# Kernel tuning notes

Hardware: AMD Instinct MI355X
Metric: run time of the kernel (lower is better)

## Reference

```python
import jax, jax.numpy as jnp
import numpy as np

B, T, D_IN, D, K, H, BAND = 4, 1536, 512, 512, 2, 8, 24
DH = D // H
ALPHA, BETA, EPS = 6.0, 0.5, 1e-5


def _ln(x, g, b):
    m = x.mean(-1, keepdims=True)
    v = ((x - m) ** 2).mean(-1, keepdims=True)
    return (x - m) / jnp.sqrt(v + EPS) * g + b


def setup_inputs() -> dict:
    key = jax.random.key(0)
    ks = jax.random.split(key, 16)
    sc = 0.02
    inp = {
        "x_m": jax.random.normal(ks[0], (B, T, D_IN), jnp.float32),
        "A": jax.random.uniform(ks[1], (B, T, K), jnp.float32),
        "W_in": jax.random.normal(ks[2], (D_IN, D), jnp.float32) * sc,
        "b_in": jnp.zeros((D,), jnp.float32),
        "ln_q_g": jnp.ones((D,), jnp.float32), "ln_q_b": jnp.zeros((D,), jnp.float32),
        "ln_kv_g": jnp.ones((D,), jnp.float32), "ln_kv_b": jnp.zeros((D,), jnp.float32),
        "Wq": jax.random.normal(ks[3], (D, D), jnp.float32) * sc,
        "bq": jnp.zeros((D,), jnp.float32),
        "Wk": jax.random.normal(ks[4], (D, D), jnp.float32) * sc,
        "bk": jnp.zeros((D,), jnp.float32),
        "Wv": jax.random.normal(ks[5], (D, D), jnp.float32) * sc,
        "bv": jnp.zeros((D,), jnp.float32),
        "Wo": jax.random.normal(ks[6], (D, D), jnp.float32) * sc,
        "bo": jnp.zeros((D,), jnp.float32),
        "ln_f_g": jnp.ones((D,), jnp.float32), "ln_f_b": jnp.zeros((D,), jnp.float32),
        "W1": jax.random.normal(ks[7], (D, 4 * D), jnp.float32) * sc,
        "b1": jnp.zeros((4 * D,), jnp.float32),
        "W2": jax.random.normal(ks[8], (4 * D, D), jnp.float32) * sc,
        "b2": jnp.zeros((D,), jnp.float32),
        "ln_s_g": jnp.ones((D,), jnp.float32), "ln_s_b": jnp.zeros((D,), jnp.float32),
        "spk_tags": jax.random.normal(ks[9], (K, D), jnp.float32) / np.sqrt(D),
    }
    return inp


def reference(x_m, A, W_in, b_in, ln_q_g, ln_q_b, ln_kv_g, ln_kv_b,
              Wq, bq, Wk, bk, Wv, bv, Wo, bo,
              ln_f_g, ln_f_b, W1, b1, W2, b2, ln_s_g, ln_s_b, spk_tags):
    X = x_m @ W_in + b_in                      # [B,T,D]
    W_hat = jax.nn.sigmoid(ALPHA * (A - BETA))  # [B,T,K] sigmoid gating

    # banded additive mask (|i-j| <= BAND allowed)
    idx = jnp.arange(T)
    allowed = jnp.abs(idx[:, None] - idx[None, :]) <= BAND
    mask = jnp.where(allowed, 0.0, -jnp.inf).astype(X.dtype)  # [T,T]

    # K/V come from the (shared) mixed memory X
    KV = _ln(X, ln_kv_g, ln_kv_b)
    k_p = (KV @ Wk + bk).reshape(B, T, H, DH)
    v_p = (KV @ Wv + bv).reshape(B, T, H, DH)

    streams = []
    for kk in range(K):
        Xk = X * W_hat[..., kk:kk + 1]
        Q = _ln(Xk, ln_q_g, ln_q_b)
        q = (Q @ Wq + bq).reshape(B, T, H, DH)
        scores = jnp.einsum('bthd,bshd->bhts', q, k_p) / np.sqrt(DH) + mask
        p = jax.nn.softmax(scores, axis=-1)
        y = jnp.einsum('bhts,bshd->bthd', p, v_p).reshape(B, T, D) @ Wo + bo
        y = Xk + y                              # residual after attention
        h = _ln(y, ln_f_g, ln_f_b)
        h = jax.nn.gelu(h @ W1 + b1, approximate=False) @ W2 + b2
        out_k = y + h + spk_tags[kk]            # ffn residual + speaker tag
        out_k = _ln(out_k, ln_s_g, ln_s_b)      # per-stream LayerNorm
        streams.append(out_k)
    return jnp.concatenate(streams, axis=1)    # [B, K*T, D]
```

## Files before the change

### kernel.cpp

```cpp
#include <hip/hip_runtime.h>
#include <hip/hip_bf16.h>
#include <math.h>

#define B_    4
#define T_    1536
#define DIN_  512
#define D_    512
#define K_    2
#define H_    8
#define BAND_ 24
#define DH_   64
#define M_    (B_*T_)
#define M2_   (2*M_)
#define ALPHA_ 6.0f
#define BETA_  0.5f
#define EPS_   1e-5f

using bf8  = __attribute__((ext_vector_type(8))) short;
using f32x4 = __attribute__((ext_vector_type(4))) float;

__device__ __forceinline__ void async_copy16(const void* g, void* l) {
  __builtin_amdgcn_global_load_lds(
      (const __attribute__((address_space(1))) unsigned int*)g,
      (__attribute__((address_space(3))) unsigned int*)l, 16, 0, 0);
}

__device__ __forceinline__ short f2bf(float v) {
  __hip_bfloat16 h = (__hip_bfloat16)v;
  return *(short*)&h;
}
__device__ __forceinline__ float bf2f(short s) {
  union { unsigned u; float f; } c;
  c.u = ((unsigned)(unsigned short)s) << 16;
  return c.f;
}
__device__ __forceinline__ int swz64(int row, int col) {
  return (col & ~63) | ((((col >> 3) ^ row) & 7) << 3) | (col & 7);
}
__device__ __forceinline__ float fast_gelu(float x) {
  const float t = fmaf(0.1029504013f, x * x, 2.3021170686f);
  const float e = __builtin_amdgcn_exp2f(x * t);
  const float r = __builtin_amdgcn_rcpf(e + 1.0f);
  return fmaf(-x, r, x);
}

template<int BM, int BN, int NI, int NJ, int FLAGS>
__global__ __launch_bounds__(256) void gemm_bt_t(
    const short* __restrict__ A, const short* __restrict__ Bt,
    const float* __restrict__ bias, const void* __restrict__ res,
    void* __restrict__ Cout, int M, int N, int Kd, int gx) {
  __shared__ short lA[BM * 64];
  __shared__ short lB[BN * 64];
  const int gy   = gridDim.x / gx;
  const int xcd  = blockIdx.x & 7;
  const int seq  = blockIdx.x >> 3;
  const int rpx  = gy >> 3;
  const int by   = xcd * rpx + seq / gx;
  const int bx   = seq % gx;
  const int tid  = threadIdx.x;
  const int wave = tid >> 6, lane = tid & 63;
  const int block_m = by * BM, block_n = bx * BN;
  const int wm = (wave & 1) * (BM / 2), wn = (wave >> 1) * (BN / 2);
  const int l15 = lane & 15, quad = lane >> 4, l7 = lane & 7;
  f32x4 acc[NI][NJ] = {};

  for (int k0 = 0; k0 < Kd; k0 += 64) {
    __syncthreads();
#pragma unroll
    for (int i = 0; i < BM / 32; ++i) {
      const int cb = wave * (BM * 2) + i * 64;
      const int c  = cb + lane;
      async_copy16(A + (size_t)(block_m + (c >> 3)) * Kd + k0 + (c & 7) * 8,
                   &lA[cb * 8]);
    }
#pragma unroll
    for (int i = 0; i < BN / 32; ++i) {
      const int cb = wave * (BN * 2) + i * 64;
      const int c  = cb + lane;
      async_copy16(Bt + (size_t)(block_n + (c >> 3)) * Kd + k0 + (c & 7) * 8,
                   &lB[cb * 8]);
    }
    __syncthreads();
#pragma unroll
    for (int ks = 0; ks < 2; ++ks) {
      bf8 af[NI], bfr[NJ];
#pragma unroll
      for (int i = 0; i < NI; ++i)
        af[i] = *(const bf8*)&lA[(wm + i * 16 + l15) * 64 + (((ks * 4 + quad) ^ l7) << 3)];
#pragma unroll
      for (int j = 0; j < NJ; ++j)
        bfr[j] = *(const bf8*)&lB[(wn + j * 16 + l15) * 64 + (((ks * 4 + quad) ^ l7) << 3)];
#pragma unroll
      for (int i = 0; i < NI; ++i)
#pragma unroll
        for (int j = 0; j < NJ; ++j)
          acc[i][j] = __builtin_amdgcn_mfma_f32_16x16x32_bf16(af[i], bfr[j], acc[i][j], 0, 0, 0);
    }
  }

#pragma unroll
  for (int i = 0; i < NI; ++i) {
    const int mbase = block_m + wm + i * 16 + (lane >> 4) * 4;
#pragma unroll
    for (int j = 0; j < NJ; ++j) {
      const int col = block_n + wn + j * 16 + l15;
      const float bb = bias[col];
#pragma unroll
      for (int r = 0; r < 4; ++r) {
        const int row = mbase + r;
        const size_t idx = (size_t)row * N + col;
        float v = acc[i][j][r] + bb;
        if constexpr (FLAGS & 8)  v += bf2f(((const short*)res)[idx]);
        if constexpr (FLAGS & 16) v += ((const float*)res)[idx];
        if constexpr (FLAGS & 1)  v = fast_gelu(v);
        if constexpr (FLAGS & 2) {
          const int oc = (FLAGS & 4) ? swz64(row, col) : col;
          ((short*)Cout)[(size_t)row * N + oc] = f2bf(v);
        } else {
          ((float*)Cout)[idx] = v;
        }
      }
    }
  }
}

__global__ __launch_bounds__(256) void tconv_k(const float* __restrict__ W,
                                               short* __restrict__ Wt, int K, int N) {
  __shared__ float s[32][33];
  const int tx = threadIdx.x & 31, ty = threadIdx.x >> 5;
  const int k0 = blockIdx.y * 32, n0 = blockIdx.x * 32;
#pragma unroll
  for (int r = 0; r < 4; ++r)
    s[ty * 4 + r][tx] = W[(size_t)(k0 + ty * 4 + r) * N + n0 + tx];
  __syncthreads();
#pragma unroll
  for (int r = 0; r < 4; ++r) {
    const int n = n0 + ty * 4 + r;
    Wt[(size_t)n * K + swz64(n, k0 + tx)] = f2bf(s[tx][ty * 4 + r]);
  }
}

__global__ void cvt_k(const float* __restrict__ x, short* __restrict__ y, int n) {
  const int i = blockIdx.x * blockDim.x + threadIdx.x;
  if (i < n) {
    const int row = i >> 9, col = i & 511;
    y[((size_t)row << 9) | swz64(row, col)] = f2bf(x[i]);
  }
}

__global__ void concat2_k(const float* __restrict__ a, const float* __restrict__ b,
                          float* __restrict__ o, int n) {
  const int i = blockIdx.x * blockDim.x + threadIdx.x;
  if (i < n) o[i] = a[i];
  else if (i < 2 * n) o[i] = b[i - n];
}

__device__ __forceinline__ float block_sum(float s, float* red, int tid) {
  red[tid] = s; __syncthreads();
  for (int o = 128; o > 0; o >>= 1) {
    if (tid < o) red[tid] += red[tid + o];
    __syncthreads();
  }
  float r = red[0];
  __syncthreads();
  return r;
}

__global__ __launch_bounds__(256) void ln_bf_k(const short* __restrict__ in,
                                               const float* __restrict__ g,
                                               const float* __restrict__ b,
                                               short* __restrict__ out) {
  __shared__ float red[256];
  const int row = blockIdx.x, tid = threadIdx.x;
  const short2 xv = *(const short2*)&in[(size_t)row * D_ + 2 * tid];
  const float v0 = bf2f(xv.x), v1 = bf2f(xv.y);
  const float mean = block_sum(v0 + v1, red, tid) * (1.0f / D_);
  const float d0 = v0 - mean, d1 = v1 - mean;
  const float var = block_sum(d0 * d0 + d1 * d1, red, tid) * (1.0f / D_);
  const float inv = rsqrtf(var + EPS_);
  const float2 gg = *(const float2*)&g[2 * tid];
  const float2 bb = *(const float2*)&b[2 * tid];
  short2 o;
  o.x = f2bf(d0 * inv * gg.x + bb.x);
  o.y = f2bf(d1 * inv * gg.y + bb.y);
  *(short2*)&out[(size_t)row * D_ + swz64(row, 2 * tid)] = o;
}

__global__ __launch_bounds__(256) void scale_ln_k(
    const short* __restrict__ X, const float* __restrict__ Ain,
    const float* __restrict__ g, const float* __restrict__ b,
    short* __restrict__ Xk, short* __restrict__ out) {
  __shared__ float red[256];
  const int row = blockIdx.x, tid = threadIdx.x;
  const int kk = row / M_, rm = row % M_;
  const float a = Ain[(size_t)rm * K_ + kk];
  const float w = __builtin_amdgcn_rcpf(1.0f + __expf(-ALPHA_ * (a - BETA_)));
  const short2 xv = *(const short2*)&X[(size_t)rm * D_ + 2 * tid];
  const float v0 = bf2f(xv.x) * w, v1 = bf2f(xv.y) * w;
  short2 xo; xo.x = f2bf(v0); xo.y = f2bf(v1);
  *(short2*)&Xk[(size_t)row * D_ + 2 * tid] = xo;
  const float mean = block_sum(v0 + v1, red, tid) * (1.0f / D_);
  const float d0 = v0 - mean, d1 = v1 - mean;
  const float var = block_sum(d0 * d0 + d1 * d1, red, tid) * (1.0f / D_);
  const float inv = rsqrtf(var + EPS_);
  const float2 gg = *(const float2*)&g[2 * tid];
  const float2 bb = *(const float2*)&b[2 * tid];
  short2 o;
  o.x = f2bf(d0 * inv * gg.x + bb.x);
  o.y = f2bf(d1 * inv * gg.y + bb.y);
  *(short2*)&out[(size_t)row * D_ + swz64(row, 2 * tid)] = o;
}

__global__ __launch_bounds__(256) void final_ln_k(
    const float* __restrict__ t2, const float* __restrict__ tags,
    const float* __restrict__ g, const float* __restrict__ b,
    float* __restrict__ out) {
  __shared__ float red[256];
  const int row = blockIdx.x, tid = threadIdx.x;
  const int kk = row / M_, rm = row % M_;
  const int bb = rm / T_, t = rm % T_;
  const size_t orow = (size_t)bb * (K_ * T_) + (size_t)kk * T_ + t;
  const float v0 = t2[(size_t)row * D_ + tid]       + tags[(size_t)kk * D_ + tid];
  const float v1 = t2[(size_t)row * D_ + tid + 256] + tags[(size_t)kk * D_ + tid + 256];
  const float mean = block_sum(v0 + v1, red, tid) * (1.0f / D_);
  const float d0 = v0 - mean, d1 = v1 - mean;
  const float var = block_sum(d0 * d0 + d1 * d1, red, tid) * (1.0f / D_);
  const float inv = rsqrtf(var + EPS_);
  out[orow * D_ + tid]       = d0 * inv * g[tid]       + b[tid];
  out[orow * D_ + tid + 256] = d1 * inv * g[tid + 256] + b[tid + 256];
}

#define QT_  64
#define KT_  (QT_ + 2 * BAND_)
#define SKQ_ 72
#define STV_ 136
__global__ __launch_bounds__(256) void attn_mfma_k(
    const short* __restrict__ q, const short* __restrict__ KVp,
    short* __restrict__ out) {
  __shared__ short sK[KT_ * SKQ_];
  __shared__ short sQ[QT_ * SKQ_];
  __shared__ short sVt[DH_ * STV_];
  __shared__ short sP[4][16 * SKQ_];
  const int t0 = blockIdx.x * QT_;
  const int h  = blockIdx.y;
  const int z  = blockIdx.z;
  const int b  = z % B_;
  const int tid = threadIdx.x;
  const int wave = tid >> 6, lane = tid & 63;
  const int rr = tid >> 5, c2 = tid & 31;

  for (int r0 = 0; r0 < KT_; r0 += 8) {
    const int r = r0 + rr;
    const int s = t0 - BAND_ + r;
    short2 kv = {0, 0}, vv = {0, 0};
    if (s >= 0 && s < T_) {
      const size_t g = (size_t)(b * T_ + s) * (2 * D_) + h * DH_ + c2 * 2;
      kv = *(const short2*)&KVp[g];
      vv = *(const short2*)&KVp[g + D_];
    }
    *(short2*)&sK[r * SKQ_ + c2 * 2] = kv;
    sVt[(c2 * 2)     * STV_ + r] = vv.x;
    sVt[(c2 * 2 + 1) * STV_ + r] = vv.y;
  }
  for (int r0 = 0; r0 < QT_; r0 += 8) {
    const int r = r0 + rr;
    const size_t g = (size_t)(z * T_ + t0 + r) * D_ + h * DH_ + c2 * 2;
    *(short2*)&sQ[r * SKQ_ + c2 * 2] = *(const short2*)&q[g];
  }
  __syncthreads();

  const int qg  = wave * 16;
  const int l15 = lane & 15, quad = lane >> 4;

  bf8 qa0 = *(const bf8*)&sQ[(qg + l15) * SKQ_ + quad * 8];
  bf8 qa1 = *(const bf8*)&sQ[(qg + l15) * SKQ_ + 32 + quad * 8];
  f32x4 acc[4];
#pragma unroll
  for (int j = 0; j < 4; ++j) {
    const bf8 kb0 = *(const bf8*)&sK[(qg + j * 16 + l15) * SKQ_ + quad * 8];
    const bf8 kb1 = *(const bf8*)&sK[(qg + j * 16 + l15) * SKQ_ + 32 + quad * 8];
    f32x4 z4 = {0.f, 0.f, 0.f, 0.f};
    acc[j] = __builtin_amdgcn_mfma_f32_16x16x32_bf16(qa0, kb0, z4, 0, 0, 0);
    acc[j] = __builtin_amdgcn_mfma_f32_16x16x32_bf16(qa1, kb1, acc[j], 0, 0, 0);
  }

#pragma unroll
  for (int reg = 0; reg < 4; ++reg) {
    const int i = quad * 4 + reg;
    float sc[4];
    float mx = -1e30f;
#pragma unroll
    for (int j = 0; j < 4; ++j) {
      const int c = j * 16 + l15;
      const int s = t0 + qg - BAND_ + c;
      const int rel = c - i;
      const bool valid = (rel >= 0) && (rel <= 2 * BAND_) && (s >= 0) && (s < T_);
      sc[j] = valid ? acc[j][reg] * 0.125f : -1e30f;
      mx = fmaxf(mx, sc[j]);
    }
    for (int o = 1; o < 16; o <<= 1) mx = fmaxf(mx, __shfl_xor(mx, o));
    float p[4], se = 0.0f;
#pragma unroll
    for (int j = 0; j < 4; ++j) {
      p[j] = (sc[j] > -1e29f) ? __expf(sc[j] - mx) : 0.0f;
      se += p[j];
    }
    for (int o = 1; o < 16; o <<= 1) se += __shfl_xor(se, o);
    const float inv = __builtin_amdgcn_rcpf(se);
#pragma unroll
    for (int j = 0; j < 4; ++j)
      sP[wave][i * SKQ_ + j * 16 + l15] = f2bf(p[j] * inv);
  }

  const bf8 pa0 = *(const bf8*)&sP[wave][l15 * SKQ_ + quad * 8];
  const bf8 pa1 = *(const bf8*)&sP[wave][l15 * SKQ_ + 32 + quad * 8];
  f32x4 oacc[4] = {};
#pragma unroll
  for (int dt = 0; dt < 4; ++dt) {
    const bf8 vb0 = *(const bf8*)&sVt[(dt * 16 + l15) * STV_ + qg + quad * 8];
    const bf8 vb1 = *(const bf8*)&sVt[(dt * 16 + l15) * STV_ + qg + 32 + quad * 8];
    oacc[dt] = __builtin_amdgcn_mfma_f32_16x16x32_bf16(pa0, vb0, oacc[dt], 0, 0, 0);
    oacc[dt] = __builtin_amdgcn_mfma_f32_16x16x32_bf16(pa1, vb1, oacc[dt], 0, 0, 0);
  }
#pragma unroll
  for (int dt = 0; dt < 4; ++dt)
#pragma unroll
    for (int reg = 0; reg < 4; ++reg) {
      const int i = quad * 4 + reg;
      const int row = t0 + qg + i;
      const int col = h * DH_ + dt * 16 + l15;
      out[(size_t)(z * T_ + row) * D_ + swz64(row, col)] = f2bf(oacc[dt][reg]);
    }
}

extern "C" void kernel_launch(void* const* d_in, const int* in_sizes, int n_in,
                              void* d_out, int out_size, void* d_ws, size_t ws_size,
                              hipStream_t stream) {
  const float* x_m    = (const float*)d_in[0];
  const float* A      = (const float*)d_in[1];
  const float* W_in   = (const float*)d_in[2];
  const float* b_in   = (const float*)d_in[3];
  const float* ln_q_g = (const float*)d_in[4];
  const float* ln_q_b = (const float*)d_in[5];
  const float* ln_kv_g= (const float*)d_in[6];
  const float* ln_kv_b= (const float*)d_in[7];
  const float* Wq     = (const float*)d_in[8];
  const float* bq     = (const float*)d_in[9];
  const float* Wk     = (const float*)d_in[10];
  const float* bk     = (const float*)d_in[11];
  const float* Wv     = (const float*)d_in[12];
  const float* bv     = (const float*)d_in[13];
  const float* Wo     = (const float*)d_in[14];
  const float* bo     = (const float*)d_in[15];
  const float* ln_f_g = (const float*)d_in[16];
  const float* ln_f_b = (const float*)d_in[17];
  const float* W1     = (const float*)d_in[18];
  const float* b1     = (const float*)d_in[19];
  const float* W2     = (const float*)d_in[20];
  const float* b2     = (const float*)d_in[21];
  const float* ln_s_g = (const float*)d_in[22];
  const float* ln_s_b = (const float*)d_in[23];
  const float* tags   = (const float*)d_in[24];
  float* out = (float*)d_out;

  const size_t MD = (size_t)M_ * D_;
  float* T2  = (float*)d_ws;
  float* bkv = T2 + 2 * MD;
  short* X    = (short*)(bkv + 1024);
  short* Xk2  = X    + MD;
  short* LNb2 = Xk2  + 2 * MD;
  short* qb2  = LNb2 + 2 * MD;
  short* KVpb = qb2  + 2 * MD;
  short* H1b  = KVpb + 2 * MD;
  short* WtIn = H1b + (size_t)M2_ * 4 * D_;
  short* WtQ  = WtIn + (size_t)D_ * DIN_;
  short* WtKV = WtQ  + (size_t)D_ * D_;
  short* WtO  = WtKV + (size_t)2 * D_ * D_;
  short* Wt1  = WtO  + (size_t)D_ * D_;
  short* Wt2  = Wt1  + (size_t)4 * D_ * D_;
  short* xb   = qb2;
  short* KVb  = LNb2;

  cvt_k<<<(M_ * DIN_ + 255) / 256, 256, 0, stream>>>(x_m, xb, M_ * DIN_);
  concat2_k<<<4, 256, 0, stream>>>(bk, bv, bkv, D_);
  tconv_k<<<dim3(D_/32,    DIN_/32),  256, 0, stream>>>(W_in, WtIn, DIN_, D_);
  tconv_k<<<dim3(D_/32,    D_/32),    256, 0, stream>>>(Wq,   WtQ,  D_,   D_);
  tconv_k<<<dim3(D_/32,    D_/32),    256, 0, stream>>>(Wk,   WtKV, D_,   D_);
  tconv_k<<<dim3(D_/32,    D_/32),    256, 0, stream>>>(Wv,   WtKV + (size_t)D_*D_, D_, D_);
  tconv_k<<<dim3(D_/32,    D_/32),    256, 0, stream>>>(Wo,   WtO,  D_,   D_);
  tconv_k<<<dim3((4*D_)/32, D_/32),   256, 0, stream>>>(W1,   Wt1,  D_,   4*D_);
  tconv_k<<<dim3(D_/32,  (4*D_)/32),  256, 0, stream>>>(W2,   Wt2,  4*D_, D_);

  gemm_bt_t<128,64,4,2, 2><<<(D_/64) * (M_/128), 256, 0, stream>>>(
      xb, WtIn, b_in, nullptr, X, M_, D_, DIN_, D_/64);
  ln_bf_k<<<M_, 256, 0, stream>>>(X, ln_kv_g, ln_kv_b, KVb);
  gemm_bt_t<128,128,4,4, 2><<<((2*D_)/128) * (M_/128), 256, 0, stream>>>(
      KVb, WtKV, bkv, nullptr, KVpb, M_, 2*D_, D_, (2*D_)/128);

  scale_ln_k<<<M2_, 256, 0, stream>>>(X, A, ln_q_g, ln_q_b, Xk2, LNb2);
  gemm_bt_t<128,128,4,4, 2><<<(D_/128) * (M2_/128), 256, 0, stream>>>(
      LNb2, WtQ, bq, nullptr, qb2, M2_, D_, D_, D_/128);
  attn_mfma_k<<<dim3(T_/QT_, H_, B_*K_), 256, 0, stream>>>(qb2, KVpb, LNb2);
  gemm_bt_t<128,128,4,4, 2|8><<<(D_/128) * (M2_/128), 256, 0, stream>>>(
      LNb2, WtO, bo, Xk2, Xk2, M2_, D_, D_, D_/128);
  ln_bf_k<<<M2_, 256, 0, stream>>>(Xk2, ln_f_g, ln_f_b, LNb2);
  gemm_bt_t<128,64,4,2, 1|2|4><<<((4*D_)/64) * (M2_/128), 256, 0, stream>>>(
      LNb2, Wt1, b1, nullptr, H1b, M2_, 4*D_, D_, (4*D_)/64);
  gemm_bt_t<128,64,4,2, 8><<<(D_/64) * (M2_/128), 256, 0, stream>>>(
      H1b, Wt2, b2, Xk2, T2, M2_, D_, 4*D_, D_/64);
  final_ln_k<<<M2_, 256, 0, stream>>>(T2, tags, ln_s_g, ln_s_b, out);
}
```

Before: 343.4 us.

## Merge prep kernels into one launch and emit bf16 FFN output with fused tag add

After: 323.0 us. 1.06x faster.

```diff
diff --git a/kernel.cpp b/kernel.cpp
--- a/kernel.cpp
+++ b/kernel.cpp
@@ -48,6 +48,7 @@
 __global__ __launch_bounds__(256) void gemm_bt_t(
     const short* __restrict__ A, const short* __restrict__ Bt,
     const float* __restrict__ bias, const void* __restrict__ res,
+    const float* __restrict__ tag2,
     void* __restrict__ Cout, int M, int N, int Kd, int gx) {
   __shared__ short lA[BM * 64];
   __shared__ short lB[BN * 64];
@@ -98,6 +99,7 @@
     }
   }
 
+  const int half = M >> 1;
 #pragma unroll
   for (int i = 0; i < NI; ++i) {
     const int mbase = block_m + wm + i * 16 + (lane >> 4) * 4;
@@ -112,6 +114,7 @@
         float v = acc[i][j][r] + bb;
         if constexpr (FLAGS & 8)  v += bf2f(((const short*)res)[idx]);
         if constexpr (FLAGS & 16) v += ((const float*)res)[idx];
+        if constexpr (FLAGS & 32) v += tag2[(row >= half ? N : 0) + col];
         if constexpr (FLAGS & 1)  v = fast_gelu(v);
         if constexpr (FLAGS & 2) {
           const int oc = (FLAGS & 4) ? swz64(row, col) : col;
@@ -124,11 +127,11 @@
   }
 }
 
-__global__ __launch_bounds__(256) void tconv_k(const float* __restrict__ W,
-                                               short* __restrict__ Wt, int K, int N) {
-  __shared__ float s[32][33];
-  const int tx = threadIdx.x & 31, ty = threadIdx.x >> 5;
-  const int k0 = blockIdx.y * 32, n0 = blockIdx.x * 32;
+__device__ __forceinline__ void tconv_tile(const float* __restrict__ W,
+                                           short* __restrict__ Wt, int K, int N,
+                                           int bx, int by, int tid, float (*s)[33]) {
+  const int tx = tid & 31, ty = tid >> 5;
+  const int k0 = by * 32, n0 = bx * 32;
 #pragma unroll
   for (int r = 0; r < 4; ++r)
     s[ty * 4 + r][tx] = W[(size_t)(k0 + ty * 4 + r) * N + n0 + tx];
@@ -140,19 +143,44 @@
   }
 }
 
-__global__ void cvt_k(const float* __restrict__ x, short* __restrict__ y, int n) {
-  const int i = blockIdx.x * blockDim.x + threadIdx.x;
-  if (i < n) {
-    const int row = i >> 9, col = i & 511;
-    y[((size_t)row << 9) | swz64(row, col)] = f2bf(x[i]);
-  }
-}
-
-__global__ void concat2_k(const float* __restrict__ a, const float* __restrict__ b,
-                          float* __restrict__ o, int n) {
-  const int i = blockIdx.x * blockDim.x + threadIdx.x;
-  if (i < n) o[i] = a[i];
-  else if (i < 2 * n) o[i] = b[i - n];
+__global__ __launch_bounds__(256) void prep_k(
+    const float* __restrict__ x_m, short* __restrict__ xb,
+    const float* __restrict__ W_in, short* __restrict__ WtIn,
+    const float* __restrict__ Wq,  short* __restrict__ WtQ,
+    const float* __restrict__ Wk,  const float* __restrict__ Wv,
+    short* __restrict__ WtKV,
+    const float* __restrict__ Wo,  short* __restrict__ WtO,
+    const float* __restrict__ W1,  short* __restrict__ Wt1,
+    const float* __restrict__ W2,  short* __restrict__ Wt2,
+    const float* __restrict__ bk,  const float* __restrict__ bv,
+    float* __restrict__ bkv) {
+  __shared__ float s[32][33];
+  const int blk = blockIdx.x, tid = threadIdx.x;
+  if (blk < 3072) {
+    const int e = (blk * 256 + tid) * 4;
+    const int row = e >> 9, col = e & 511;
+    const float4 v = *(const float4*)&x_m[e];
+    short4 o;
+    o.x = f2bf(v.x); o.y = f2bf(v.y); o.z = f2bf(v.z); o.w = f2bf(v.w);
+    *(short4*)&xb[((size_t)row << 9) | swz64(row, col)] = o;
+  } else if (blk < 3328) {
+    const int t = blk - 3072; tconv_tile(W_in, WtIn, DIN_, D_, t & 15, t >> 4, tid, s);
+  } else if (blk < 3584) {
+    const int t = blk - 3328; tconv_tile(Wq, WtQ, D_, D_, t & 15, t >> 4, tid, s);
+  } else if (blk < 3840) {
+    const int t = blk - 3584; tconv_tile(Wk, WtKV, D_, D_, t & 15, t >> 4, tid, s);
+  } else if (blk < 4096) {
+    const int t = blk - 3840; tconv_tile(Wv, WtKV + (size_t)D_ * D_, D_, D_, t & 15, t >> 4, tid, s);
+  } else if (blk < 4352) {
+    const int t = blk - 4096; tconv_tile(Wo, WtO, D_, D_, t & 15, t >> 4, tid, s);
+  } else if (blk < 5376) {
+    const int t = blk - 4352; tconv_tile(W1, Wt1, D_, 4 * D_, t & 63, t >> 6, tid, s);
+  } else if (blk < 6400) {
+    const int t = blk - 5376; tconv_tile(W2, Wt2, 4 * D_, D_, t & 15, t >> 4, tid, s);
+  } else {
+    const int i = (blk - 6400) * 256 + tid;
+    bkv[i] = (i < D_) ? bk[i] : bv[i - D_];
+  }
 }
 
 __device__ __forceinline__ float block_sum(float s, float* red, int tid) {
@@ -212,22 +240,25 @@
 }
 
 __global__ __launch_bounds__(256) void final_ln_k(
-    const float* __restrict__ t2, const float* __restrict__ tags,
-    const float* __restrict__ g, const float* __restrict__ b,
-    float* __restrict__ out) {
+    const short* __restrict__ t2, const float* __restrict__ g,
+    const float* __restrict__ b, float* __restrict__ out) {
   __shared__ float red[256];
   const int row = blockIdx.x, tid = threadIdx.x;
   const int kk = row / M_, rm = row % M_;
-  const int bb = rm / T_, t = rm % T_;
-  const size_t orow = (size_t)bb * (K_ * T_) + (size_t)kk * T_ + t;
-  const float v0 = t2[(size_t)row * D_ + tid]       + tags[(size_t)kk * D_ + tid];
-  const float v1 = t2[(size_t)row * D_ + tid + 256] + tags[(size_t)kk * D_ + tid + 256];
+  const int bb_ = rm / T_, t = rm % T_;
+  const size_t orow = (size_t)bb_ * (K_ * T_) + (size_t)kk * T_ + t;
+  const short2 xv = *(const short2*)&t2[(size_t)row * D_ + 2 * tid];
+  const float v0 = bf2f(xv.x), v1 = bf2f(xv.y);
   const float mean = block_sum(v0 + v1, red, tid) * (1.0f / D_);
   const float d0 = v0 - mean, d1 = v1 - mean;
   const float var = block_sum(d0 * d0 + d1 * d1, red, tid) * (1.0f / D_);
   const float inv = rsqrtf(var + EPS_);
-  out[orow * D_ + tid]       = d0 * inv * g[tid]       + b[tid];
-  out[orow * D_ + tid + 256] = d1 * inv * g[tid + 256] + b[tid + 256];
+  const float2 gg = *(const float2*)&g[2 * tid];
+  const float2 bb = *(const float2*)&b[2 * tid];
+  float2 o;
+  o.x = d0 * inv * gg.x + bb.x;
+  o.y = d1 * inv * gg.y + bb.y;
+  *(float2*)&out[orow * D_ + 2 * tid] = o;
 }
 
 #define QT_  64
@@ -364,14 +395,14 @@
   float* out = (float*)d_out;
 
   const size_t MD = (size_t)M_ * D_;
-  float* T2  = (float*)d_ws;
-  float* bkv = T2 + 2 * MD;
+  float* bkv = (float*)d_ws;
   short* X    = (short*)(bkv + 1024);
   short* Xk2  = X    + MD;
   short* LNb2 = Xk2  + 2 * MD;
   short* qb2  = LNb2 + 2 * MD;
   short* KVpb = qb2  + 2 * MD;
-  short* H1b  = KVpb + 2 * MD;
+  short* T2b  = KVpb + 2 * MD;
+  short* H1b  = T2b  + 2 * MD;
   short* WtIn = H1b + (size_t)M2_ * 4 * D_;
   short* WtQ  = WtIn + (size_t)D_ * DIN_;
   short* WtKV = WtQ  + (size_t)D_ * D_;
@@ -381,32 +412,25 @@
   short* xb   = qb2;
   short* KVb  = LNb2;
 
-  cvt_k<<<(M_ * DIN_ + 255) / 256, 256, 0, stream>>>(x_m, xb, M_ * DIN_);
-  concat2_k<<<4, 256, 0, stream>>>(bk, bv, bkv, D_);
-  tconv_k<<<dim3(D_/32,    DIN_/32),  256, 0, stream>>>(W_in, WtIn, DIN_, D_);
-  tconv_k<<<dim3(D_/32,    D_/32),    256, 0, stream>>>(Wq,   WtQ,  D_,   D_);
-  tconv_k<<<dim3(D_/32,    D_/32),    256, 0, stream>>>(Wk,   WtKV, D_,   D_);
-  tconv_k<<<dim3(D_/32,    D_/32),    256, 0, stream>>>(Wv,   WtKV + (size_t)D_*D_, D_, D_);
-  tconv_k<<<dim3(D_/32,    D_/32),    256, 0, stream>>>(Wo,   WtO,  D_,   D_);
-  tconv_k<<<dim3((4*D_)/32, D_/32),   256, 0, stream>>>(W1,   Wt1,  D_,   4*D_);
-  tconv_k<<<dim3(D_/32,  (4*D_)/32),  256, 0, stream>>>(W2,   Wt2,  4*D_, D_);
+  prep_k<<<6404, 256, 0, stream>>>(x_m, xb, W_in, WtIn, Wq, WtQ, Wk, Wv, WtKV,
+                                   Wo, WtO, W1, Wt1, W2, Wt2, bk, bv, bkv);
 
   gemm_bt_t<128,64,4,2, 2><<<(D_/64) * (M_/128), 256, 0, stream>>>(
-      xb, WtIn, b_in, nullptr, X, M_, D_, DIN_, D_/64);
+      xb, WtIn, b_in, nullptr, nullptr, X, M_, D_, DIN_, D_/64);
   ln_bf_k<<<M_, 256, 0, stream>>>(X, ln_kv_g, ln_kv_b, KVb);
   gemm_bt_t<128,128,4,4, 2><<<((2*D_)/128) * (M_/128), 256, 0, stream>>>(
-      KVb, WtKV, bkv, nullptr, KVpb, M_, 2*D_, D_, (2*D_)/128);
+      KVb, WtKV, bkv, nullptr, nullptr, KVpb, M_, 2*D_, D_, (2*D_)/128);
 
   scale_ln_k<<<M2_, 256, 0, stream>>>(X, A, ln_q_g, ln_q_b, Xk2, LNb2);
   gemm_bt_t<128,128,4,4, 2><<<(D_/128) * (M2_/128), 256, 0, stream>>>(
-      LNb2, WtQ, bq, nullptr, qb2, M2_, D_, D_, D_/128);
+      LNb2, WtQ, bq, nullptr, nullptr, qb2, M2_, D_, D_, D_/128);
   attn_mfma_k<<<dim3(T_/QT_, H_, B_*K_), 256, 0, stream>>>(qb2, KVpb, LNb2);
   gemm_bt_t<128,128,4,4, 2|8><<<(D_/128) * (M2_/128), 256, 0, stream>>>(
-      LNb2, WtO, bo, Xk2, Xk2, M2_, D_, D_, D_/128);
+      LNb2, WtO, bo, Xk2, nullptr, Xk2, M2_, D_, D_, D_/128);
   ln_bf_k<<<M2_, 256, 0, stream>>>(Xk2, ln_f_g, ln_f_b, LNb2);
   gemm_bt_t<128,64,4,2, 1|2|4><<<((4*D_)/64) * (M2_/128), 256, 0, stream>>>(
-      LNb2, Wt1, b1, nullptr, H1b, M2_, 4*D_, D_, (4*D_)/64);
-  gemm_bt_t<128,64,4,2, 8><<<(D_/64) * (M2_/128), 256, 0, stream>>>(
-      H1b, Wt2, b2, Xk2, T2, M2_, D_, 4*D_, D_/64);
-  final_ln_k<<<M2_, 256, 0, stream>>>(T2, tags, ln_s_g, ln_s_b, out);
-}
+      LNb2, Wt1, b1, nullptr, nullptr, H1b, M2_, 4*D_, D_, (4*D_)/64);
+  gemm_bt_t<128,64,4,2, 2|8|32><<<(D_/64) * (M2_/128), 256, 0, stream>>>(
+      H1b, Wt2, b2, Xk2, tags, T2b, M2_, D_, 4*D_, D_/64);
+  final_ln_k<<<M2_, 256, 0, stream>>>(T2b, ln_s_g, ln_s_b, out);
+}
```
